# Performance work log

Hardware: AMD Instinct MI355X
Metric: run time of the kernel (lower is better)

Reference implementation:

```python
import jax, jax.numpy as jnp
import numpy as np

B, S, E, A = 4, 2048, 1024, 1024

def setup_inputs() -> dict:
    key = jax.random.key(0)
    ks = jax.random.split(key, 6)
    scale = 1.0 / np.sqrt(E)
    return {
        "query": jax.random.normal(ks[0], (B, S, E), jnp.float32),
        "key": jax.random.normal(ks[1], (B, S, E), jnp.float32),
        "value": jax.random.normal(ks[2], (B, S, E), jnp.float32),
        "Wq": jax.random.normal(ks[3], (E, A), jnp.float32) * scale,
        "bq": jnp.zeros((A,), jnp.float32),
        "Wk": jax.random.normal(ks[4], (E, A), jnp.float32) * scale,
        "bk": jnp.zeros((A,), jnp.float32),
        "Wv": jax.random.normal(ks[5], (E, A), jnp.float32) * scale,
        "bv": jnp.zeros((A,), jnp.float32),
    }

def reference(query, key, value, Wq, bq, Wk, bk, Wv, bv):
    # QKV linear projections: [B,S,E] @ [E,A] + [A]
    q = jnp.einsum("bse,ea->bsa", query, Wq) + bq
    k = jnp.einsum("bse,ea->bsa", key, Wk) + bk
    v = jnp.einsum("bse,ea->bsa", value, Wv) + bv
    # scaled dot-product attention (no mask, single head)
    inv_sqrt_d = 1.0 / jnp.sqrt(jnp.asarray(A, q.dtype))
    scores = jnp.einsum("bqa,bka->bqk", q, k) * inv_sqrt_d  # [B,S,S]
    probs = jax.nn.softmax(scores, axis=-1)
    return jnp.einsum("bqk,bka->bqa", probs, v)
```

## Files before the change

### kernel.cpp

```cpp
#include <hip/hip_runtime.h>

typedef unsigned short u16;
typedef __attribute__((ext_vector_type(4))) float f32x4;
typedef __attribute__((ext_vector_type(8))) short s16x8;
typedef __attribute__((ext_vector_type(8))) unsigned short u16x8;
typedef __attribute__((ext_vector_type(4))) unsigned short u16x4;

__device__ __forceinline__ u16 f2b(float x) {
  union { float f; unsigned u; } v; v.f = x;
  unsigned r = v.u + 0x7fffu + ((v.u >> 16) & 1u);
  return (u16)(r >> 16);
}
__device__ __forceinline__ float b2f(u16 x) {
  union { unsigned u; float f; } v; v.u = ((unsigned)x) << 16;
  return v.f;
}

__global__ __launch_bounds__(256) void cast3_f32_bf16(const float* __restrict__ s0,
                                                      const float* __restrict__ s1,
                                                      const float* __restrict__ s2,
                                                      u16* __restrict__ dst, long n4) {
  const float* src = (blockIdx.y == 0) ? s0 : ((blockIdx.y == 1) ? s1 : s2);
  long i = blockIdx.x * 256 + threadIdx.x;
  if (i >= n4) return;
  float4 f = ((const float4*)src)[i];
  u16x4 o;
  o.x = f2b(f.x); o.y = f2b(f.y); o.z = f2b(f.z); o.w = f2b(f.w);
  ((u16x4*)(dst + blockIdx.y * n4 * 4))[i] = o;
}

__global__ __launch_bounds__(256) void transpose_cast_w3(const float* __restrict__ w0,
                                                         const float* __restrict__ w1,
                                                         const float* __restrict__ w2,
                                                         u16* __restrict__ Wt, int E_, int A_) {
  __shared__ float tile[32][33];
  const float* W = (blockIdx.z == 0) ? w0 : ((blockIdx.z == 1) ? w1 : w2);
  u16* dst = Wt + (long)blockIdx.z * E_ * A_;
  int a0 = blockIdx.x * 32, e0 = blockIdx.y * 32;
  int tx = threadIdx.x & 31, ty = threadIdx.x >> 5;
  for (int i = ty; i < 32; i += 8) tile[i][tx] = W[(long)(e0 + i) * A_ + a0 + tx];
  __syncthreads();
  for (int i = ty; i < 32; i += 8) dst[(long)(a0 + i) * E_ + e0 + tx] = f2b(tile[tx][i]);
}

template<int MODE, bool KSPLIT>
__global__ __launch_bounds__(256, 2)
void gemm4w(const u16* __restrict__ Ag, const u16* __restrict__ Bg,
            const float* __restrict__ b0, const float* __restrict__ b1,
            const float* __restrict__ b2, void* __restrict__ Cg,
            int gn, int KLEN, int LDA, int LDB, int N, float scale,
            long sA, long sB, long sC, long sKh,
            u16* __restrict__ VtG, long vtB, int vtS) {
  __shared__ __align__(128) char ldsc[73728];
  const int t = threadIdx.x;
  const int w = t >> 6, l = t & 63;

  const int nwg = gridDim.x;
  const int Lb = blockIdx.x;
  const int chunk = nwg >> 3;
  const int id = (Lb & 7) * chunk + (Lb >> 3);
  const int im = id / gn, in = id % gn;
  const int m0 = im * 128, n0 = in * 256;
  int z = blockIdx.z, kh = 0;
  if (KSPLIT) { kh = z & 1; z >>= 1; }
  const float* bias = (z == 0) ? b0 : ((z == 1) ? b1 : b2);

  const u16* Ab = Ag + (long)z * sA + (long)m0 * LDA + (long)kh * KLEN;
  const u16* Bb = Bg + (long)z * sB + (long)n0 * LDB + (long)kh * KLEN;

  const long soA = (long)(t >> 2) * LDA + (long)(((t & 3) ^ ((t >> 3) & 3)) << 3);
  const long soB = (long)(t >> 2) * LDB + (long)(((t & 3) ^ ((t >> 3) & 3)) << 3);
  const int d16 = t * 16;

  const int cbR = (((l >> 4) ^ ((l >> 1) & 3)) << 4);
  const int aB = ((l & 15) << 6) + cbR;
  const int bB = 8192 + (w << 12) + ((l & 15) << 6) + cbR;

  f32x4 acc[8][4] = {};
  s16x8 af[8], bf[4];
  const int NTt = KLEN >> 5;

#define GLD(SRC, DST)                                                                        \
  __builtin_amdgcn_global_load_lds(                                                         \
      (const __attribute__((address_space(1))) unsigned int*)(SRC),                         \
      (__attribute__((address_space(3))) unsigned int*)(DST), 16, 0, 0)

#define STG(TT, SBASE) do {                                                                  \
    const u16* _sa = Ab + ((long)(TT) << 5) + soA;                                           \
    GLD(_sa,                   ldsc + (SBASE) + d16);                                        \
    GLD(_sa + (long)64 * LDA,  ldsc + (SBASE) + 4096 + d16);                                 \
    const u16* _sv = Bb + ((long)(TT) << 5) + soB;                                           \
    GLD(_sv,                   ldsc + (SBASE) + 8192 + d16);                                 \
    GLD(_sv + (long)64 * LDB,  ldsc + (SBASE) + 12288 + d16);                                \
    GLD(_sv + (long)128 * LDB, ldsc + (SBASE) + 16384 + d16);                                \
    GLD(_sv + (long)192 * LDB, ldsc + (SBASE) + 20480 + d16);                                \
  } while (0)

  STG(0, 0);
  STG(1, 24576);
  asm volatile("s_waitcnt vmcnt(6)" ::: "memory");
  __builtin_amdgcn_s_barrier();

  int cb = 0, sb = 49152;
  for (int tt = 0; tt < NTt; ++tt) {
#pragma unroll
    for (int i = 0; i < 8; ++i) af[i] = *(const s16x8*)(ldsc + cb + aB + (i << 10));
#pragma unroll
    for (int j = 0; j < 4; ++j) bf[j] = *(const s16x8*)(ldsc + cb + bB + (j << 10));
    if (tt + 2 < NTt) STG(tt + 2, sb);
    __builtin_amdgcn_s_setprio(1);
#pragma unroll
    for (int i = 0; i < 8; ++i)
#pragma unroll
      for (int j = 0; j < 4; ++j)
        acc[i][j] = __builtin_amdgcn_mfma_f32_16x16x32_bf16(af[i], bf[j], acc[i][j], 0, 0, 0);
    __builtin_amdgcn_s_setprio(0);
    if (tt + 2 < NTt)      asm volatile("s_waitcnt vmcnt(6)" ::: "memory");
    else if (tt + 1 < NTt) asm volatile("s_waitcnt vmcnt(0)" ::: "memory");
    __builtin_amdgcn_s_barrier();
    cb += 24576; if (cb >= 73728) cb = 0;
    sb += 24576; if (sb >= 73728) sb = 0;
  }
#undef STG
#undef GLD

  float bj[4];
#pragma unroll
  for (int j = 0; j < 4; ++j) {
    int col = n0 + w * 64 + j * 16 + (l & 15);
    bj[j] = bias ? bias[col] : 0.0f;
  }

  if (MODE == 0 && VtG != nullptr && z == 2) {
    const int b = m0 / vtS, smod = m0 % vtS;
    u16* vbase = VtG + (long)b * vtB + smod + ((l >> 4) << 2);
#pragma unroll
    for (int i8 = 0; i8 < 8; ++i8)
#pragma unroll
      for (int j = 0; j < 4; ++j) {
        int col = n0 + w * 64 + j * 16 + (l & 15);
        u16x4 o;
#pragma unroll
        for (int r = 0; r < 4; ++r) o[r] = f2b(acc[i8][j][r] * scale + bj[j]);
        *(u16x4*)(vbase + (long)col * vtS + i8 * 16) = o;
      }
  } else {
    char* Cz = (char*)Cg;
    long rbase = (long)z * sC + (KSPLIT ? (long)kh * sKh : 0) +
                 (long)(m0 + ((l >> 4) << 2)) * N + n0 + w * 64 + (l & 15);
#pragma unroll
    for (int i8 = 0; i8 < 8; ++i8)
#pragma unroll
      for (int j = 0; j < 4; ++j)
#pragma unroll
        for (int r = 0; r < 4; ++r) {
          float v = acc[i8][j][r] * scale + bj[j];
          if (MODE == 1) v = __expf(v);
          long ro = rbase + (long)(i8 * 16 + r) * N + j * 16;
          if (MODE == 2) ((float*)Cz)[ro] = v;
          else           ((u16*)Cz)[ro] = f2b(v);
        }
  }
}

__device__ __forceinline__ float wred_sum(float x) {
  for (int o = 32; o > 0; o >>= 1) x += __shfl_xor(x, o);
  return x;
}

__global__ __launch_bounds__(256) void rowsum_bf16(const u16* __restrict__ Pm,
                                                   float* __restrict__ Z, int ncols) {
  long row = blockIdx.x;
  const u16x8* p8 = (const u16x8*)(Pm + row * (long)ncols);
  int t = threadIdx.x, wave = t >> 6, lane = t & 63;
  u16x8 a = p8[t];
  float s = 0.f;
#pragma unroll
  for (int i = 0; i < 8; i++) s += b2f(a[i]);
  s = wred_sum(s);
  __shared__ float red[4];
  if (lane == 0) red[wave] = s;
  __syncthreads();
  if (t == 0) Z[row] = red[0] + red[1] + red[2] + red[3];
}

__global__ __launch_bounds__(256) void add2z_f32(const float* __restrict__ a,
                                                 const float* __restrict__ b,
                                                 const float* __restrict__ Z,
                                                 float* __restrict__ o, long n4) {
  long i = blockIdx.x * 256 + threadIdx.x;
  if (i >= n4) return;
  float inv = 1.0f / Z[i >> 8];
  float4 x = ((const float4*)a)[i];
  float4 y = ((const float4*)b)[i];
  float4 r;
  r.x = (x.x + y.x) * inv; r.y = (x.y + y.y) * inv;
  r.z = (x.z + y.z) * inv; r.w = (x.w + y.w) * inv;
  ((float4*)o)[i] = r;
}

extern "C" void kernel_launch(void* const* d_in, const int* in_sizes, int n_in,
                              void* d_out, int out_size, void* d_ws, size_t ws_size,
                              hipStream_t stream) {
  const float* query = (const float*)d_in[0];
  const float* key_  = (const float*)d_in[1];
  const float* value = (const float*)d_in[2];
  const float* Wq = (const float*)d_in[3];
  const float* bq = (const float*)d_in[4];
  const float* Wk = (const float*)d_in[5];
  const float* bk = (const float*)d_in[6];
  const float* Wv = (const float*)d_in[7];
  const float* bv = (const float*)d_in[8];

  constexpr int B = 4, S = 2048, E = 1024, A = 1024;
  constexpr long MB = 1024 * 1024;
  char* ws = (char*)d_ws;
  u16* Qb  = (u16*)(ws + 0 * MB);
  u16* Kb  = (u16*)(ws + 16 * MB);
  u16* Vt  = (u16*)(ws + 48 * MB);
  u16* Pt  = (u16*)(ws + 64 * MB);
  u16* Xq  = (u16*)(ws + 96 * MB);
  u16* WqT = (u16*)(ws + 144 * MB);
  float* Z   = (float*)(ws + 150 * MB);
  float* Cp0 = (float*)(ws + 0 * MB);

  const long n = (long)B * S * E;
  const long n4 = n / 4;
  dim3 blk(256);

  cast3_f32_bf16<<<dim3(n4 / 256, 3), blk, 0, stream>>>(query, key_, value, Xq, n4);

  transpose_cast_w3<<<dim3(A / 32, E / 32, 3), blk, 0, stream>>>(Wq, Wk, Wv, WqT, E, A);

  gemm4w<0, false><<<dim3(256, 1, 3), blk, 0, stream>>>(
      Xq, WqT, bq, bk, bv, Qb, 4, E, E, E, A, 1.0f,
      (long)8 * MB, (long)1 * MB, (long)8 * MB, 0,
      Vt, (long)A * S, S);

  gemm4w<1, false><<<dim3(128, 1, 4), blk, 0, stream>>>(
      Qb, Kb, nullptr, nullptr, nullptr, Pt, 8, A, A, A, S, 0.03125f,
      (long)S * A, (long)S * A, (long)S * S, 0, nullptr, 0, 1);

  rowsum_bf16<<<dim3(B * S), blk, 0, stream>>>(Pt, Z, S);

  gemm4w<2, true><<<dim3(64, 1, 8), blk, 0, stream>>>(
      Pt, Vt, nullptr, nullptr, nullptr, Cp0, 4, 1024, S, S, A, 1.0f,
      (long)S * S, (long)S * A, (long)S * A, (long)24 * MB, nullptr, 0, 1);

  const long o4 = (long)B * S * A / 4;
  add2z_f32<<<dim3(o4 / 256), blk, 0, stream>>>(Cp0, (const float*)(ws + 96 * MB), Z,
                                                (float*)d_out, o4);
}
```

Baseline: 319.1 us.

## Fuse softmax row sums and normalization into GEMM epilogues, drop split-K

Row sums of exp(scores) are now accumulated by atomics in the QK^T GEMM epilogue, which removes the separate rowsum kernel. The PV GEMM drops split-K in favour of a BN=128 tile template with the full K loop, and it divides by the row sum in its epilogue, which removes the partial-sum buffers and the add/normalize kernel. A memset of Z is added up front. The cost is float atomics and a longer K loop per block.

```diff
diff --git a/kernel.cpp b/kernel.cpp
--- a/kernel.cpp
+++ b/kernel.cpp
@@ -43,15 +43,18 @@
   for (int i = ty; i < 32; i += 8) dst[(long)(a0 + i) * E_ + e0 + tx] = f2b(tile[tx][i]);
 }
 
-template<int MODE, bool KSPLIT>
+template<int MODE, int BN>
 __global__ __launch_bounds__(256, 2)
 void gemm4w(const u16* __restrict__ Ag, const u16* __restrict__ Bg,
             const float* __restrict__ b0, const float* __restrict__ b1,
             const float* __restrict__ b2, void* __restrict__ Cg,
             int gn, int KLEN, int LDA, int LDB, int N, float scale,
-            long sA, long sB, long sC, long sKh,
-            u16* __restrict__ VtG, long vtB, int vtS) {
-  __shared__ __align__(128) char ldsc[73728];
+            long sA, long sB, long sC,
+            u16* __restrict__ VtG, long vtB, int vtS, float* __restrict__ Zp) {
+  constexpr int J = BN / 64;
+  constexpr int WN = BN / 4;
+  constexpr int SLOT = 8192 + BN * 64;
+  __shared__ __align__(128) char ldsc[3 * SLOT];
   const int t = threadIdx.x;
   const int w = t >> 6, l = t & 63;
 
@@ -60,13 +63,12 @@
   const int chunk = nwg >> 3;
   const int id = (Lb & 7) * chunk + (Lb >> 3);
   const int im = id / gn, in = id % gn;
-  const int m0 = im * 128, n0 = in * 256;
-  int z = blockIdx.z, kh = 0;
-  if (KSPLIT) { kh = z & 1; z >>= 1; }
+  const int m0 = im * 128, n0 = in * BN;
+  const int z = blockIdx.z;
   const float* bias = (z == 0) ? b0 : ((z == 1) ? b1 : b2);
 
-  const u16* Ab = Ag + (long)z * sA + (long)m0 * LDA + (long)kh * KLEN;
-  const u16* Bb = Bg + (long)z * sB + (long)n0 * LDB + (long)kh * KLEN;
+  const u16* Ab = Ag + (long)z * sA + (long)m0 * LDA;
+  const u16* Bb = Bg + (long)z * sB + (long)n0 * LDB;
 
   const long soA = (long)(t >> 2) * LDA + (long)(((t & 3) ^ ((t >> 3) & 3)) << 3);
   const long soB = (long)(t >> 2) * LDB + (long)(((t & 3) ^ ((t >> 3) & 3)) << 3);
@@ -74,10 +76,10 @@
 
   const int cbR = (((l >> 4) ^ ((l >> 1) & 3)) << 4);
   const int aB = ((l & 15) << 6) + cbR;
-  const int bB = 8192 + (w << 12) + ((l & 15) << 6) + cbR;
-
-  f32x4 acc[8][4] = {};
-  s16x8 af[8], bf[4];
+  const int bB = 8192 + w * (WN * 64) + ((l & 15) << 6) + cbR;
+
+  f32x4 acc[8][J] = {};
+  s16x8 af[8], bf[J];
   const int NTt = KLEN >> 5;
 
 #define GLD(SRC, DST)                                                                        \
@@ -92,42 +94,50 @@
     const u16* _sv = Bb + ((long)(TT) << 5) + soB;                                           \
     GLD(_sv,                   ldsc + (SBASE) + 8192 + d16);                                 \
     GLD(_sv + (long)64 * LDB,  ldsc + (SBASE) + 12288 + d16);                                \
-    GLD(_sv + (long)128 * LDB, ldsc + (SBASE) + 16384 + d16);                                \
-    GLD(_sv + (long)192 * LDB, ldsc + (SBASE) + 20480 + d16);                                \
+    if (BN == 256) {                                                                         \
+      GLD(_sv + (long)128 * LDB, ldsc + (SBASE) + 16384 + d16);                              \
+      GLD(_sv + (long)192 * LDB, ldsc + (SBASE) + 20480 + d16);                              \
+    }                                                                                        \
   } while (0)
 
+#define VMW_OPS() do {                                                                       \
+    if (BN == 256) asm volatile("s_waitcnt vmcnt(6)" ::: "memory");                          \
+    else           asm volatile("s_waitcnt vmcnt(4)" ::: "memory");                          \
+  } while (0)
+
   STG(0, 0);
-  STG(1, 24576);
-  asm volatile("s_waitcnt vmcnt(6)" ::: "memory");
+  STG(1, SLOT);
+  VMW_OPS();
   __builtin_amdgcn_s_barrier();
 
-  int cb = 0, sb = 49152;
+  int cb = 0, sb = 2 * SLOT;
   for (int tt = 0; tt < NTt; ++tt) {
 #pragma unroll
     for (int i = 0; i < 8; ++i) af[i] = *(const s16x8*)(ldsc + cb + aB + (i << 10));
 #pragma unroll
-    for (int j = 0; j < 4; ++j) bf[j] = *(const s16x8*)(ldsc + cb + bB + (j << 10));
+    for (int j = 0; j < J; ++j) bf[j] = *(const s16x8*)(ldsc + cb + bB + (j << 10));
     if (tt + 2 < NTt) STG(tt + 2, sb);
     __builtin_amdgcn_s_setprio(1);
 #pragma unroll
     for (int i = 0; i < 8; ++i)
 #pragma unroll
-      for (int j = 0; j < 4; ++j)
+      for (int j = 0; j < J; ++j)
         acc[i][j] = __builtin_amdgcn_mfma_f32_16x16x32_bf16(af[i], bf[j], acc[i][j], 0, 0, 0);
     __builtin_amdgcn_s_setprio(0);
-    if (tt + 2 < NTt)      asm volatile("s_waitcnt vmcnt(6)" ::: "memory");
+    if (tt + 2 < NTt)      VMW_OPS();
     else if (tt + 1 < NTt) asm volatile("s_waitcnt vmcnt(0)" ::: "memory");
     __builtin_amdgcn_s_barrier();
-    cb += 24576; if (cb >= 73728) cb = 0;
-    sb += 24576; if (sb >= 73728) sb = 0;
+    cb += SLOT; if (cb >= 3 * SLOT) cb = 0;
+    sb += SLOT; if (sb >= 3 * SLOT) sb = 0;
   }
 #undef STG
 #undef GLD
-
-  float bj[4];
-#pragma unroll
-  for (int j = 0; j < 4; ++j) {
-    int col = n0 + w * 64 + j * 16 + (l & 15);
+#undef VMW_OPS
+
+  float bj[J];
+#pragma unroll
+  for (int j = 0; j < J; ++j) {
+    int col = n0 + w * WN + j * 16 + (l & 15);
     bj[j] = bias ? bias[col] : 0.0f;
   }
 
@@ -137,66 +147,59 @@
 #pragma unroll
     for (int i8 = 0; i8 < 8; ++i8)
 #pragma unroll
-      for (int j = 0; j < 4; ++j) {
-        int col = n0 + w * 64 + j * 16 + (l & 15);
+      for (int j = 0; j < J; ++j) {
+        int col = n0 + w * WN + j * 16 + (l & 15);
         u16x4 o;
 #pragma unroll
         for (int r = 0; r < 4; ++r) o[r] = f2b(acc[i8][j][r] * scale + bj[j]);
         *(u16x4*)(vbase + (long)col * vtS + i8 * 16) = o;
       }
+  } else if (MODE == 1) {
+    u16* Cz = (u16*)Cg;
+    long rbase = (long)z * sC + (long)(m0 + ((l >> 4) << 2)) * N + n0 + w * WN + (l & 15);
+#pragma unroll
+    for (int i8 = 0; i8 < 8; ++i8) {
+      float s4[4] = {0.f, 0.f, 0.f, 0.f};
+#pragma unroll
+      for (int j = 0; j < J; ++j)
+#pragma unroll
+        for (int r = 0; r < 4; ++r) {
+          float v = __expf(acc[i8][j][r] * scale);
+          Cz[rbase + (long)(i8 * 16 + r) * N + j * 16] = f2b(v);
+          s4[r] += v;
+        }
+#pragma unroll
+      for (int r = 0; r < 4; ++r) {
+        s4[r] += __shfl_xor(s4[r], 1);
+        s4[r] += __shfl_xor(s4[r], 2);
+        s4[r] += __shfl_xor(s4[r], 4);
+        s4[r] += __shfl_xor(s4[r], 8);
+      }
+      if ((l & 15) == 0) {
+        long zrow = (long)z * N + m0 + i8 * 16 + ((l >> 4) << 2);
+#pragma unroll
+        for (int r = 0; r < 4; ++r) atomicAdd(&Zp[zrow + r], s4[r]);
+      }
+    }
   } else {
     char* Cz = (char*)Cg;
-    long rbase = (long)z * sC + (KSPLIT ? (long)kh * sKh : 0) +
-                 (long)(m0 + ((l >> 4) << 2)) * N + n0 + w * 64 + (l & 15);
+    long rbase = (long)z * sC + (long)(m0 + ((l >> 4) << 2)) * N + n0 + w * WN + (l & 15);
 #pragma unroll
     for (int i8 = 0; i8 < 8; ++i8)
 #pragma unroll
-      for (int j = 0; j < 4; ++j)
+      for (int j = 0; j < J; ++j)
 #pragma unroll
         for (int r = 0; r < 4; ++r) {
           float v = acc[i8][j][r] * scale + bj[j];
-          if (MODE == 1) v = __expf(v);
           long ro = rbase + (long)(i8 * 16 + r) * N + j * 16;
-          if (MODE == 2) ((float*)Cz)[ro] = v;
-          else           ((u16*)Cz)[ro] = f2b(v);
+          if (MODE == 2) {
+            long zrow = (long)z * vtS + m0 + i8 * 16 + ((l >> 4) << 2) + r;
+            ((float*)Cz)[ro] = v * (1.0f / Zp[zrow]);
+          } else {
+            ((u16*)Cz)[ro] = f2b(v);
+          }
         }
   }
-}
-
-__device__ __forceinline__ float wred_sum(float x) {
-  for (int o = 32; o > 0; o >>= 1) x += __shfl_xor(x, o);
-  return x;
-}
-
-__global__ __launch_bounds__(256) void rowsum_bf16(const u16* __restrict__ Pm,
-                                                   float* __restrict__ Z, int ncols) {
-  long row = blockIdx.x;
-  const u16x8* p8 = (const u16x8*)(Pm + row * (long)ncols);
-  int t = threadIdx.x, wave = t >> 6, lane = t & 63;
-  u16x8 a = p8[t];
-  float s = 0.f;
-#pragma unroll
-  for (int i = 0; i < 8; i++) s += b2f(a[i]);
-  s = wred_sum(s);
-  __shared__ float red[4];
-  if (lane == 0) red[wave] = s;
-  __syncthreads();
-  if (t == 0) Z[row] = red[0] + red[1] + red[2] + red[3];
-}
-
-__global__ __launch_bounds__(256) void add2z_f32(const float* __restrict__ a,
-                                                 const float* __restrict__ b,
-                                                 const float* __restrict__ Z,
-                                                 float* __restrict__ o, long n4) {
-  long i = blockIdx.x * 256 + threadIdx.x;
-  if (i >= n4) return;
-  float inv = 1.0f / Z[i >> 8];
-  float4 x = ((const float4*)a)[i];
-  float4 y = ((const float4*)b)[i];
-  float4 r;
-  r.x = (x.x + y.x) * inv; r.y = (x.y + y.y) * inv;
-  r.z = (x.z + y.z) * inv; r.w = (x.w + y.w) * inv;
-  ((float4*)o)[i] = r;
 }
 
 extern "C" void kernel_launch(void* const* d_in, const int* in_sizes, int n_in,
@@ -221,33 +224,28 @@
   u16* Pt  = (u16*)(ws + 64 * MB);
   u16* Xq  = (u16*)(ws + 96 * MB);
   u16* WqT = (u16*)(ws + 144 * MB);
-  float* Z   = (float*)(ws + 150 * MB);
-  float* Cp0 = (float*)(ws + 0 * MB);
+  float* Z = (float*)(ws + 150 * MB);
 
   const long n = (long)B * S * E;
   const long n4 = n / 4;
   dim3 blk(256);
 
+  hipMemsetAsync(Z, 0, (size_t)B * S * sizeof(float), stream);
+
   cast3_f32_bf16<<<dim3(n4 / 256, 3), blk, 0, stream>>>(query, key_, value, Xq, n4);
 
   transpose_cast_w3<<<dim3(A / 32, E / 32, 3), blk, 0, stream>>>(Wq, Wk, Wv, WqT, E, A);
 
-  gemm4w<0, false><<<dim3(256, 1, 3), blk, 0, stream>>>(
+  gemm4w<0, 256><<<dim3(256, 1, 3), blk, 0, stream>>>(
       Xq, WqT, bq, bk, bv, Qb, 4, E, E, E, A, 1.0f,
-      (long)8 * MB, (long)1 * MB, (long)8 * MB, 0,
-      Vt, (long)A * S, S);
-
-  gemm4w<1, false><<<dim3(128, 1, 4), blk, 0, stream>>>(
+      (long)8 * MB, (long)1 * MB, (long)8 * MB,
+      Vt, (long)A * S, S, nullptr);
+
+  gemm4w<1, 256><<<dim3(128, 1, 4), blk, 0, stream>>>(
       Qb, Kb, nullptr, nullptr, nullptr, Pt, 8, A, A, A, S, 0.03125f,
-      (long)S * A, (long)S * A, (long)S * S, 0, nullptr, 0, 1);
-
-  rowsum_bf16<<<dim3(B * S), blk, 0, stream>>>(Pt, Z, S);
-
-  gemm4w<2, true><<<dim3(64, 1, 8), blk, 0, stream>>>(
-      Pt, Vt, nullptr, nullptr, nullptr, Cp0, 4, 1024, S, S, A, 1.0f,
-      (long)S * S, (long)S * A, (long)S * A, (long)24 * MB, nullptr, 0, 1);
-
-  const long o4 = (long)B * S * A / 4;
-  add2z_f32<<<dim3(o4 / 256), blk, 0, stream>>>(Cp0, (const float*)(ws + 96 * MB), Z,
-                                                (float*)d_out, o4);
-}
+      (long)S * A, (long)S * A, (long)S * S, nullptr, 0, 1, Z);
+
+  gemm4w<2, 128><<<dim3(128, 1, 4), blk, 0, stream>>>(
+      Pt, Vt, nullptr, nullptr, nullptr, (float*)d_out, 8, S, S, S, A, 1.0f,
+      (long)S * S, (long)S * A, (long)S * A, nullptr, 0, S, Z);
+}
```

Measured after the change: 305.6 us. 4.2% less time.
